# Performance work log

Hardware: AMD Instinct MI355X
Metric: run time of the kernel (lower is better)

Reference implementation:

```python
import jax, jax.numpy as jnp
import numpy as np

NUM_HEADS = 32
NUM_KV_HEADS = 8
NUM_GROUPS = NUM_HEADS // NUM_KV_HEADS  # 4
HEAD_DIM = 64
HIDDEN = 2048
ROPE_THETA = 10000.0


def rotate_half(x):
    half = x.shape[-1] // 2
    x1, x2 = x[..., :half], x[..., half:]
    return jnp.concatenate([-x2, x1], axis=-1)


def rope_cos_sin(seq_len, dtype):
    inv_freq = 1.0 / (ROPE_THETA ** (jnp.arange(0, HEAD_DIM, 2, dtype=jnp.float32) / HEAD_DIM))
    pos = jnp.arange(seq_len, dtype=jnp.float32)
    freqs = jnp.outer(pos, inv_freq)          # [S, HEAD_DIM/2]
    emb = jnp.concatenate([freqs, freqs], axis=-1)  # [S, HEAD_DIM]
    return jnp.cos(emb).astype(dtype), jnp.sin(emb).astype(dtype)


def setup_inputs() -> dict:
    key = jax.random.key(0)
    k0, k1, k2, k3, k4 = jax.random.split(key, 5)
    B, S = 2, 2048
    scale = 0.02
    return {
        "hidden_states": jax.random.normal(k0, (B, S, HIDDEN), dtype=jnp.float32),
        "Wq": jax.random.normal(k1, (NUM_HEADS * HEAD_DIM, HIDDEN), dtype=jnp.float32) * scale,
        "Wk": jax.random.normal(k2, (NUM_KV_HEADS * HEAD_DIM, HIDDEN), dtype=jnp.float32) * scale,
        "Wv": jax.random.normal(k3, (NUM_KV_HEADS * HEAD_DIM, HIDDEN), dtype=jnp.float32) * scale,
        "Wo": jax.random.normal(k4, (HIDDEN, NUM_HEADS * HEAD_DIM), dtype=jnp.float32) * scale,
    }


def reference(hidden_states, Wq, Wk, Wv, Wo):
    B, S, _ = hidden_states.shape
    # projections (nn.Linear: x @ W.T)
    q = (hidden_states @ Wq.T).reshape(B, S, NUM_HEADS, HEAD_DIM).transpose(0, 2, 1, 3)
    k = (hidden_states @ Wk.T).reshape(B, S, NUM_KV_HEADS, HEAD_DIM).transpose(0, 2, 1, 3)
    v = (hidden_states @ Wv.T).reshape(B, S, NUM_KV_HEADS, HEAD_DIM).transpose(0, 2, 1, 3)

    cos, sin = rope_cos_sin(S, q.dtype)  # [S, HEAD_DIM]
    cos = cos[None, None]                # [1,1,S,HEAD_DIM]
    sin = sin[None, None]
    q = q * cos + rotate_half(q) * sin
    k = k * cos + rotate_half(k) * sin

    # GQA: repeat kv heads to match query heads (repeat_interleave on head dim)
    k = jnp.repeat(k, NUM_GROUPS, axis=1)  # [B, NUM_HEADS, S, HEAD_DIM]
    v = jnp.repeat(v, NUM_GROUPS, axis=1)

    scale = 1.0 / jnp.sqrt(jnp.asarray(HEAD_DIM, dtype=q.dtype))
    scores = jnp.einsum('bhqd,bhkd->bhqk', q, k) * scale  # [B,H,S,S]
    causal = jnp.tril(jnp.ones((S, S), dtype=bool))
    scores = jnp.where(causal[None, None], scores, jnp.asarray(-jnp.inf, dtype=scores.dtype))
    attn = jax.nn.softmax(scores, axis=-1)
    out = jnp.einsum('bhqk,bhkd->bhqd', attn, v)           # [B,H,S,D]
    out = out.transpose(0, 2, 1, 3).reshape(B, S, NUM_HEADS * HEAD_DIM)
    return out @ Wo.T
```

## Files before the change

kernel.cpp:

```cpp
#include <hip/hip_runtime.h>

#define S_LEN 2048
#define BATCH 2
#define NH 32
#define NKV 8
#define HD 64
#define HID 2048
#define NTOK (BATCH * S_LEN)
#define NQKV 3072
#define SC_Q 0.18033688011112042f

typedef __attribute__((ext_vector_type(8))) __bf16 bf16x8;
typedef __attribute__((ext_vector_type(4))) float f32x4;
typedef __attribute__((ext_vector_type(4))) float f32x4v;
typedef __attribute__((ext_vector_type(4))) ushort u16x4;

__device__ inline ushort f2b(float f) {
    union { float f; unsigned u; } x{f};
    unsigned r = (x.u + 0x7fff + ((x.u >> 16) & 1)) >> 16;
    return (ushort)r;
}
__device__ inline float b2f(ushort u) {
    union { unsigned u; float f; } x{(unsigned)u << 16};
    return x.f;
}
__device__ inline float ex2(float x) { return __builtin_amdgcn_exp2f(x); }

__global__ __launch_bounds__(256) void cvt_all(const float* __restrict__ hidden,
                                               const float* __restrict__ Wq,
                                               const float* __restrict__ Wk,
                                               const float* __restrict__ Wv,
                                               const float* __restrict__ Wo,
                                               ushort* __restrict__ hb,
                                               ushort* __restrict__ wqkv,
                                               ushort* __restrict__ wo) {
    for (int bid = blockIdx.x; bid < 18432; bid += gridDim.x) {
        const float* src;
        ushort* dst;
        int off;
        if (bid < 8192)        { src = hidden; dst = hb;                              off = bid; }
        else if (bid < 12288)  { src = Wq;     dst = wqkv;                            off = bid - 8192; }
        else if (bid < 13312)  { src = Wk;     dst = wqkv + (size_t)2048 * 2048;      off = bid - 12288; }
        else if (bid < 14336)  { src = Wv;     dst = wqkv + (size_t)2560 * 2048;      off = bid - 13312; }
        else                   { src = Wo;     dst = wo;                              off = bid - 14336; }
        size_t i = (size_t)off * 256 + threadIdx.x;
        f32x4v v = __builtin_nontemporal_load((const f32x4v*)src + i);
        u16x4 o = {f2b(v[0]), f2b(v[1]), f2b(v[2]), f2b(v[3])};
        *((u16x4*)dst + i) = o;
    }
}

__device__ inline void gl_lds16(const void* g, void* l) {
    __builtin_amdgcn_global_load_lds((const __attribute__((address_space(1))) void*)g,
                                     (__attribute__((address_space(3))) void*)l, 16, 0, 0);
}

__global__ __launch_bounds__(512, 2) void gemmQKV(const ushort* __restrict__ A,
                                                  const ushort* __restrict__ B,
                                                  ushort* __restrict__ Qd,
                                                  ushort* __restrict__ Kd,
                                                  ushort* __restrict__ Vd,
                                                  int M, int N, int K) {
    constexpr int CF = 3;
    constexpr int ABYTES = 256 * 64 * 2;
    constexpr int BBYTES = 192 * 64 * 2;
    __shared__ __align__(16) char lds[2][ABYTES + BBYTES];
    const int tid = threadIdx.x, lane = tid & 63, w = tid >> 6;
    const int wm = w >> 2, wn = w & 3, l15 = lane & 15, lg = lane >> 4;

    const int nbx = gridDim.x;
    int lid = blockIdx.y * nbx + blockIdx.x;
    const int cpx = (nbx * gridDim.y) >> 3;
    int swzb = (lid & 7) * cpx + (lid >> 3);
    const int m0 = (swzb / nbx) * 256, n0 = (swzb % nbx) * (CF * 64);

    const int srow = tid >> 3;
    const int scol = ((tid & 7) ^ (srow & 7)) * 8;
    const ushort* Ag = A + (size_t)(m0 + srow) * K + scol;
    const ushort* Bg = B + (size_t)(n0 + srow) * K + scol;

    auto stage = [&](int buf, int k0) {
        char* base = &lds[buf][0];
#pragma unroll
        for (int j = 0; j < CF; j++)
            gl_lds16(Bg + (size_t)(j * 64) * K + k0, base + ABYTES + (j * 64 + w * 8) * 128);
        gl_lds16(Ag + k0,                        base + (0 * 64 + w * 8) * 128);
        gl_lds16(Ag + (size_t)(2 * 64) * K + k0, base + (2 * 64 + w * 8) * 128);
        gl_lds16(Ag + (size_t)(1 * 64) * K + k0, base + (1 * 64 + w * 8) * 128);
        gl_lds16(Ag + (size_t)(3 * 64) * K + k0, base + (3 * 64 + w * 8) * 128);
    };

    f32x4 acc[8][CF] = {};

    stage(0, 0);

    const int NT = K >> 6;
    const int sw = (l15 & 7) * 16;
    const int po0 = (lg * 16) ^ sw, po1 = (64 + lg * 16) ^ sw;

    for (int t = 0; t < NT; ++t) {
        const char* pa = &lds[t & 1][0] + (wm * 128 + l15) * 128;
        const char* pb = &lds[t & 1][ABYTES] + (wn * CF * 16 + l15) * 128;

        asm volatile("s_waitcnt vmcnt(2)" ::: "memory");
        __builtin_amdgcn_s_barrier();
        __builtin_amdgcn_sched_barrier(0);
        if (t + 1 < NT) stage((t + 1) & 1, (t + 1) << 6);
        __builtin_amdgcn_sched_barrier(0);

        bf16x8 bf_[2][CF];
#pragma unroll
        for (int j = 0; j < CF; j++) {
            bf_[0][j] = *(const bf16x8*)(pb + j * 2048 + po0);
            bf_[1][j] = *(const bf16x8*)(pb + j * 2048 + po1);
        }
        bf16x8 a_[2][4];
#pragma unroll
        for (int i = 0; i < 4; i++) {
            a_[0][i] = *(const bf16x8*)(pa + i * 2048 + po0);
            a_[1][i] = *(const bf16x8*)(pa + i * 2048 + po1);
        }
        __builtin_amdgcn_s_setprio(1);
#pragma unroll
        for (int ks = 0; ks < 2; ks++)
#pragma unroll
            for (int i = 0; i < 4; i++)
#pragma unroll
                for (int j = 0; j < CF; j++)
                    acc[i][j] = __builtin_amdgcn_mfma_f32_16x16x32_bf16(a_[ks][i], bf_[ks][j], acc[i][j], 0, 0, 0);
        __builtin_amdgcn_s_setprio(0);

        if (t < NT - 1) asm volatile("s_waitcnt vmcnt(7)" ::: "memory");
        else            asm volatile("s_waitcnt vmcnt(0)" ::: "memory");
        __builtin_amdgcn_s_barrier();
        __builtin_amdgcn_sched_barrier(0);

        bf16x8 c_[2][4];
#pragma unroll
        for (int i = 0; i < 4; i++) {
            c_[0][i] = *(const bf16x8*)(pa + (4 + i) * 2048 + po0);
            c_[1][i] = *(const bf16x8*)(pa + (4 + i) * 2048 + po1);
        }
        __builtin_amdgcn_s_setprio(1);
#pragma unroll
        for (int ks = 0; ks < 2; ks++)
#pragma unroll
            for (int i = 0; i < 4; i++)
#pragma unroll
                for (int j = 0; j < CF; j++)
                    acc[4 + i][j] = __builtin_amdgcn_mfma_f32_16x16x32_bf16(c_[ks][i], bf_[ks][j], acc[4 + i][j], 0, 0, 0);
        __builtin_amdgcn_s_setprio(0);
    }

    const int mr = m0 + wm * 128 + lg * 4;
#pragma unroll
    for (int j = 0; j < CF; j++) {
        int cb = n0 + wn * CF * 16 + j * 16;
        ushort* dst;
        int dstride, colb;
        if (cb < 2048)      { dst = Qd; dstride = 2048; colb = cb + l15; }
        else if (cb < 2560) { dst = Kd; dstride = 512;  colb = cb - 2048 + l15; }
        else                { dst = Vd; dstride = 512;  colb = cb - 2560 + l15; }
#pragma unroll
        for (int i = 0; i < 8; i++)
#pragma unroll
            for (int r = 0; r < 4; r++)
                dst[(size_t)(mr + i * 16 + r) * dstride + colb] = f2b(acc[i][j][r]);
    }
}

__global__ __launch_bounds__(512, 2) void gemmO(const ushort* __restrict__ A,
                                                const ushort* __restrict__ B,
                                                float* __restrict__ C,
                                                int M, int N, int K) {
    constexpr int ABYTES = 128 * 64 * 2;
    constexpr int BBYTES = 256 * 64 * 2;
    __shared__ __align__(16) char lds[2][ABYTES + BBYTES];
    const int tid = threadIdx.x, lane = tid & 63, w = tid >> 6;
    const int wm = w >> 2, wn = w & 3, l15 = lane & 15, lg = lane >> 4;

    const int nbx = gridDim.x;
    int lid = blockIdx.y * nbx + blockIdx.x;
    const int cpx = (nbx * gridDim.y) >> 3;
    int swzb = (lid & 7) * cpx + (lid >> 3);
    const int m0 = (swzb / nbx) * 128, n0 = (swzb % nbx) * 256;

    const int srow = tid >> 3;
    const int scol = ((tid & 7) ^ (srow & 7)) * 8;
    const ushort* Ag = A + (size_t)(m0 + srow) * K + scol;
    const ushort* Bg = B + (size_t)(n0 + srow) * K + scol;

    auto stage = [&](int buf, int k0) {
        char* base = &lds[buf][0];
        gl_lds16(Ag + k0,                   base + (w * 8) * 128);
        gl_lds16(Ag + (size_t)64 * K + k0,  base + (64 + w * 8) * 128);
#pragma unroll
        for (int j = 0; j < 4; j++)
            gl_lds16(Bg + (size_t)(j * 64) * K + k0, base + ABYTES + (j * 64 + w * 8) * 128);
    };

    f32x4 acc[4][4] = {};

    stage(0, 0);
    stage(1, 64);

    const int NT = K >> 6;
    const int sw = (l15 & 7) * 16;
    const int po0 = (lg * 16) ^ sw, po1 = (64 + lg * 16) ^ sw;

    for (int t = 0; t < NT; ++t) {
        if (t < NT - 1) asm volatile("s_waitcnt vmcnt(6)" ::: "memory");
        else            asm volatile("s_waitcnt vmcnt(0)" ::: "memory");
        __builtin_amdgcn_s_barrier();
        __builtin_amdgcn_sched_barrier(0);

        const char* pa = &lds[t & 1][0] + (wm * 64 + l15) * 128;
        const char* pb = &lds[t & 1][ABYTES] + (wn * 64 + l15) * 128;

        bf16x8 a_[2][4], b_[2][4];
#pragma unroll
        for (int i = 0; i < 4; i++) {
            a_[0][i] = *(const bf16x8*)(pa + i * 2048 + po0);
            a_[1][i] = *(const bf16x8*)(pa + i * 2048 + po1);
            b_[0][i] = *(const bf16x8*)(pb + i * 2048 + po0);
            b_[1][i] = *(const bf16x8*)(pb + i * 2048 + po1);
        }
        __builtin_amdgcn_s_setprio(1);
#pragma unroll
        for (int ks = 0; ks < 2; ks++)
#pragma unroll
            for (int i = 0; i < 4; i++)
#pragma unroll
                for (int j = 0; j < 4; j++)
                    acc[i][j] = __builtin_amdgcn_mfma_f32_16x16x32_bf16(a_[ks][i], b_[ks][j], acc[i][j], 0, 0, 0);
        __builtin_amdgcn_s_setprio(0);

        __builtin_amdgcn_sched_barrier(0);
        __builtin_amdgcn_s_barrier();
        __builtin_amdgcn_sched_barrier(0);
        if (t + 2 < NT) stage(t & 1, (t + 2) << 6);
    }

    const int mr = m0 + wm * 64 + lg * 4, nc = n0 + wn * 64 + l15;
#pragma unroll
    for (int i = 0; i < 4; i++)
#pragma unroll
        for (int j = 0; j < 4; j++)
#pragma unroll
            for (int r = 0; r < 4; r++)
                C[(size_t)(mr + i * 16 + r) * N + nc + j * 16] = acc[i][j][r];
}

__global__ __launch_bounds__(256) void rope_k(ushort* __restrict__ Kb) {
    int idx = blockIdx.x * 256 + threadIdx.x;
    int t = idx >> 5, rem = idx & 31;
    int hh = rem >> 2, q8 = rem & 3;
    float pos = (float)(t & (S_LEN - 1));
    ushort* base = Kb + (size_t)t * 512 + hh * 64 + q8 * 8;
    ushort4 v0 = *(ushort4*)base, v1 = *(ushort4*)(base + 4);
    ushort4 u0 = *(ushort4*)(base + 32), u1 = *(ushort4*)(base + 36);
    ushort lo[8] = {v0.x, v0.y, v0.z, v0.w, v1.x, v1.y, v1.z, v1.w};
    ushort hi[8] = {u0.x, u0.y, u0.z, u0.w, u1.x, u1.y, u1.z, u1.w};
#pragma unroll
    for (int e = 0; e < 8; e++) {
        float f = ex2(-(float)(q8 * 8 + e) * 0.4152410118609203f);
        float sv, cv;
        __sincosf(pos * f, &sv, &cv);
        float x1 = b2f(lo[e]), x2 = b2f(hi[e]);
        lo[e] = f2b(x1 * cv - x2 * sv);
        hi[e] = f2b(x2 * cv + x1 * sv);
    }
    *(ushort4*)base        = make_ushort4(lo[0], lo[1], lo[2], lo[3]);
    *(ushort4*)(base + 4)  = make_ushort4(lo[4], lo[5], lo[6], lo[7]);
    *(ushort4*)(base + 32) = make_ushort4(hi[0], hi[1], hi[2], hi[3]);
    *(ushort4*)(base + 36) = make_ushort4(hi[4], hi[5], hi[6], hi[7]);
}

__global__ __launch_bounds__(256) void transpose_v(const ushort* __restrict__ V,
                                                   ushort* __restrict__ Vt) {
    __shared__ ushort tile[32][33];
    int bz = blockIdx.z, b = bz >> 3, kvh = bz & 7;
    int s0 = blockIdx.x * 32, d0 = blockIdx.y * 32;
    int tx = threadIdx.x & 31, ty = threadIdx.x >> 5;
#pragma unroll
    for (int i = 0; i < 4; i++)
        tile[ty + i * 8][tx] = V[(size_t)(b * S_LEN + s0 + ty + i * 8) * 512 + kvh * 64 + d0 + tx];
    __syncthreads();
#pragma unroll
    for (int i = 0; i < 4; i++)
        Vt[((size_t)((b * 8 + kvh) * 64 + d0 + ty + i * 8)) * S_LEN + s0 + tx] = tile[tx][ty + i * 8];
}

__global__ __launch_bounds__(256) void attn_k(const ushort* __restrict__ Q,
                                              const ushort* __restrict__ Kc,
                                              const ushort* __restrict__ Vt,
                                              ushort* __restrict__ O) {
    __shared__ __align__(16) ushort K_lds[3][4096];
    __shared__ __align__(16) ushort V_lds[3][4096];
    const int lane = threadIdx.x & 63, w = threadIdx.x >> 6;
    const int l15 = lane & 15, lg = lane >> 4;

    int lid = blockIdx.y * 8 + blockIdx.x;
    int swz = (lid & 7) * 64 + (lid >> 3);
    const int ps = swz & 7;
    const int bh = swz >> 3;
    const int b = bh >> 5, h = bh & 31, kvh = h >> 2;

    const ushort* kSrc[2];
    const ushort* vSrc[2];
    int dstU[2];
#pragma unroll
    for (int j = 0; j < 2; j++) {
        int u = w * 2 + j;
        int row = u * 8 + (lane >> 3);
        int po = (lane & 7) * 16;
        int fr = ((row & 3) | (((row >> 3) & 1) << 2)) << 4;
        int dus = (po ^ fr) >> 1;
        kSrc[j] = Kc + (size_t)(b * S_LEN + row) * 512 + kvh * 64 + dus;
        vSrc[j] = Vt + ((size_t)((b * 8 + kvh) * 64 + row)) * S_LEN + dus;
        dstU[j] = u * 512;
    }

    int fr_k = ((l15 & 3) | (((l15 >> 2) & 1) << 2)) << 4;
    int kbase = 1024 * (l15 >> 2) + 128 * (l15 & 3) + ((lg * 16) ^ (fr_k & 48));
    int k6 = (fr_k >> 6) & 1;
    int kb0 = kbase + 64 * k6, kb1 = kbase + 64 * (1 - k6);
    int fr_v = ((l15 & 3) | (((l15 >> 3) & 1) << 2)) << 4;
    int vbase = 128 * l15 + ((lg * 16) ^ (fr_v & 48));
    int v6 = (fr_v >> 6) & 1;
    int vb0 = vbase + 64 * v6, vb1 = vbase + 64 * (1 - v6);

    bf16x8 onesf;
#pragma unroll
    for (int i = 0; i < 8; i++) onesf[i] = (__bf16)1.0f;

    auto ropeq = [&](bf16x8& q0, bf16x8& q1, int qrow) {
        float pos = (float)qrow;
#pragma unroll
        for (int e = 0; e < 8; e++) {
            float f = ex2(-(float)(lg * 8 + e) * 0.4152410118609203f);
            float sv, cv;
            __sincosf(pos * f, &sv, &cv);
            float x1 = (float)q0[e], x2 = (float)q1[e];
            q0[e] = (__bf16)((x1 * cv - x2 * sv) * SC_Q);
            q1[e] = (__bf16)((x2 * cv + x1 * sv) * SC_Q);
        }
    };

    for (int half = 0; half < 2; ++half) {
        const int pp = half ? (15 - ps) : ps;
        const int q0A = pp * 128 + w * 16, q0B = q0A + 64;
        const int qrowA = q0A + l15, qrowB = q0B + l15;
        const int ktA = 2 * pp, ktB = 2 * pp + 1;

        const ushort* qpA = Q + (size_t)(b * S_LEN + qrowA) * HID + h * 64 + lg * 8;
        const ushort* qpB = Q + (size_t)(b * S_LEN + qrowB) * HID + h * 64 + lg * 8;
        bf16x8 qfA0 = *(const bf16x8*)qpA, qfA1 = *(const bf16x8*)(qpA + 32);
        bf16x8 qfB0 = *(const bf16x8*)qpB, qfB1 = *(const bf16x8*)(qpB + 32);
        ropeq(qfA0, qfA1, qrowA);
        ropeq(qfB0, qfB1, qrowB);
        asm volatile("s_waitcnt vmcnt(0)" ::: "memory");

        f32x4 aoA[4] = {}, aoB[4] = {};
        f32x4 lsumA = {}, lsumB = {};

        int i0 = 0, i1 = 1, i2 = 2;
#pragma unroll
        for (int j = 0; j < 2; j++) {
            gl_lds16(kSrc[j], &K_lds[0][dstU[j]]);
            gl_lds16(vSrc[j], &V_lds[0][dstU[j]]);
        }
#pragma unroll
        for (int j = 0; j < 2; j++) {
            gl_lds16(kSrc[j] + (size_t)64 * 512, &K_lds[1][dstU[j]]);
            gl_lds16(vSrc[j] + 64, &V_lds[1][dstU[j]]);
        }

        for (int kt = 0; kt <= ktB; ++kt) {
            const int kn = kt << 6;
            if (kt < ktB) asm volatile("s_waitcnt vmcnt(4)" ::: "memory");
            else          asm volatile("s_waitcnt vmcnt(0)" ::: "memory");
            __builtin_amdgcn_s_barrier();

            if (kt + 2 <= ktB) {
                const int kn2 = kn + 128;
#pragma unroll
                for (int j = 0; j < 2; j++) {
                    gl_lds16(kSrc[j] + (size_t)kn2 * 512, &K_lds[i2][dstU[j]]);
                    gl_lds16(vSrc[j] + kn2, &V_lds[i2][dstU[j]]);
                }
            }

            const char* Kt = (const char*)&K_lds[i0][0];
            const char* Vl = (const char*)&V_lds[i0][0];
            const bool aAct = (kt <= ktA);

            bf16x8 kf0[4], kf1[4];
#pragma unroll
            for (int kc = 0; kc < 4; kc++) {
                const int kcst = 4096 * (kc >> 1) + 512 * (kc & 1);
                kf0[kc] = *(const bf16x8*)(Kt + kb0 + kcst);
                kf1[kc] = *(const bf16x8*)(Kt + kb1 + kcst);
            }

            f32x4 sB[4], sA[4];
#pragma unroll
            for (int kc = 0; kc < 4; kc++) {
                f32x4 z = {};
                z = __builtin_amdgcn_mfma_f32_16x16x32_bf16(kf0[kc], qfB0, z, 0, 0, 0);
                z = __builtin_amdgcn_mfma_f32_16x16x32_bf16(kf1[kc], qfB1, z, 0, 0, 0);
                sB[kc] = z;
            }
            if (aAct) {
#pragma unroll
                for (int kc = 0; kc < 4; kc++) {
                    f32x4 z = {};
                    z = __builtin_amdgcn_mfma_f32_16x16x32_bf16(kf0[kc], qfA0, z, 0, 0, 0);
                    z = __builtin_amdgcn_mfma_f32_16x16x32_bf16(kf1[kc], qfA1, z, 0, 0, 0);
                    sA[kc] = z;
                }
            }

            if (kt == ktB) {
#pragma unroll
                for (int kc = 0; kc < 4; kc++)
#pragma unroll
                    for (int r = 0; r < 4; r++) {
                        int kv = kn + ((kc >> 1) << 5) + (lg << 3) + ((kc & 1) << 2) + r;
                        sB[kc][r] = (kv <= qrowB) ? sB[kc][r] : -INFINITY;
                    }
            }
            if (kt == ktA) {
#pragma unroll
                for (int kc = 0; kc < 4; kc++)
#pragma unroll
                    for (int r = 0; r < 4; r++) {
                        int kv = kn + ((kc >> 1) << 5) + (lg << 3) + ((kc & 1) << 2) + r;
                        sA[kc][r] = (kv <= qrowA) ? sA[kc][r] : -INFINITY;
                    }
            }

            bf16x8 pB0, pB1, pA0, pA1;
#pragma unroll
            for (int r = 0; r < 4; r++) {
                pB0[r]     = (__bf16)ex2(sB[0][r]);
                pB0[4 + r] = (__bf16)ex2(sB[1][r]);
                pB1[r]     = (__bf16)ex2(sB[2][r]);
                pB1[4 + r] = (__bf16)ex2(sB[3][r]);
            }
            if (aAct) {
#pragma unroll
                for (int r = 0; r < 4; r++) {
                    pA0[r]     = (__bf16)ex2(sA[0][r]);
                    pA0[4 + r] = (__bf16)ex2(sA[1][r]);
                    pA1[r]     = (__bf16)ex2(sA[2][r]);
                    pA1[4 + r] = (__bf16)ex2(sA[3][r]);
                }
            }

            lsumB = __builtin_amdgcn_mfma_f32_16x16x32_bf16(pB0, onesf, lsumB, 0, 0, 0);
            lsumB = __builtin_amdgcn_mfma_f32_16x16x32_bf16(pB1, onesf, lsumB, 0, 0, 0);
            if (aAct) {
                lsumA = __builtin_amdgcn_mfma_f32_16x16x32_bf16(pA0, onesf, lsumA, 0, 0, 0);
                lsumA = __builtin_amdgcn_mfma_f32_16x16x32_bf16(pA1, onesf, lsumA, 0, 0, 0);
            }

#pragma unroll
            for (int dt = 0; dt < 4; dt++) {
                bf16x8 vf0 = *(const bf16x8*)(Vl + vb0 + dt * 2048);
                bf16x8 vf1 = *(const bf16x8*)(Vl + vb1 + dt * 2048);
                aoB[dt] = __builtin_amdgcn_mfma_f32_16x16x32_bf16(pB0, vf0, aoB[dt], 0, 0, 0);
                aoB[dt] = __builtin_amdgcn_mfma_f32_16x16x32_bf16(pB1, vf1, aoB[dt], 0, 0, 0);
                if (aAct) {
                    aoA[dt] = __builtin_amdgcn_mfma_f32_16x16x32_bf16(pA0, vf0, aoA[dt], 0, 0, 0);
                    aoA[dt] = __builtin_amdgcn_mfma_f32_16x16x32_bf16(pA1, vf1, aoA[dt], 0, 0, 0);
                }
            }

            int t = i0; i0 = i1; i1 = i2; i2 = t;
        }

        float invA[4], invB[4];
#pragma unroll
        for (int r = 0; r < 4; r++) { invA[r] = 1.0f / lsumA[r]; invB[r] = 1.0f / lsumB[r]; }
        ushort* obA = O + (size_t)(b * S_LEN + q0A + lg * 4) * HID + h * 64 + l15;
        ushort* obB = O + (size_t)(b * S_LEN + q0B + lg * 4) * HID + h * 64 + l15;
#pragma unroll
        for (int dt = 0; dt < 4; dt++)
#pragma unroll
            for (int r = 0; r < 4; r++) {
                union { __bf16 h; ushort u; } cA{(__bf16)(aoA[dt][r] * invA[r])};
                union { __bf16 h; ushort u; } cB{(__bf16)(aoB[dt][r] * invB[r])};
                obA[(size_t)r * HID + dt * 16] = cA.u;
                obB[(size_t)r * HID + dt * 16] = cB.u;
            }

        __builtin_amdgcn_s_barrier();
    }
}

extern "C" void kernel_launch(void* const* d_in, const int* in_sizes, int n_in,
                              void* d_out, int out_size, void* d_ws, size_t ws_size,
                              hipStream_t stream) {
    const float* hidden = (const float*)d_in[0];
    const float* Wq = (const float*)d_in[1];
    const float* Wk = (const float*)d_in[2];
    const float* Wv = (const float*)d_in[3];
    const float* Wo = (const float*)d_in[4];

    char* ws = (char*)d_ws;
    size_t off = 0;
    auto alloc = [&](size_t bytes) -> void* {
        void* p = ws + off;
        off += (bytes + 255) & ~(size_t)255;
        return p;
    };
    ushort* hb   = (ushort*)alloc((size_t)NTOK * HID * 2);
    ushort* wqkv = (ushort*)alloc((size_t)NQKV * 2048 * 2);
    ushort* wo   = (ushort*)alloc((size_t)2048 * 2048 * 2);
    ushort* Qb   = (ushort*)alloc((size_t)NTOK * 2048 * 2);
    ushort* Kb   = (ushort*)alloc((size_t)NTOK * 512 * 2);
    ushort* Vb   = (ushort*)alloc((size_t)NTOK * 512 * 2);
    ushort* Vtb  = (ushort*)alloc((size_t)NTOK * 512 * 2);
    ushort* AO   = (ushort*)alloc((size_t)NTOK * 2048 * 2);

    cvt_all<<<2304, 256, 0, stream>>>(hidden, Wq, Wk, Wv, Wo, hb, wqkv, wo);

    gemmQKV<<<dim3(16, 16), 512, 0, stream>>>(hb, wqkv, Qb, Kb, Vb, NTOK, NQKV, 2048);

    rope_k<<<(NTOK * 32) / 256, 256, 0, stream>>>(Kb);

    transpose_v<<<dim3(S_LEN / 32, 2, BATCH * NKV), 256, 0, stream>>>(Vb, Vtb);

    attn_k<<<dim3(8, BATCH * NH), 256, 0, stream>>>(Qb, Kb, Vtb, AO);

    gemmO<<<dim3(8, 32), 512, 0, stream>>>(AO, wo, (float*)d_out, NTOK, 2048, 2048);
}
```

Measured before the change: 166.8 us.

## Restructure GEMM pipelines: single-phase QKV loop and triple-buffered O-projection

The QKV GEMM main loop drops its split two-phase schedule, which waited on partial A loads. It now waits for all loads, issues the next stage's prefetch, and runs all 8 A-row fragments in one MFMA block. This takes one barrier out of each iteration but raises register pressure (16 A fragments live) and removes the overlap of the second A half's load with compute. The O-projection GEMM moves from two to three rotating LDS buffers, issuing the t+2 prefetch right after the top barrier and dropping the end-of-iteration barrier, at the cost of more LDS per block that may reduce occupancy.

```diff
diff --git a/kernel.cpp b/kernel.cpp
--- a/kernel.cpp
+++ b/kernel.cpp
@@ -84,10 +84,9 @@
 #pragma unroll
         for (int j = 0; j < CF; j++)
             gl_lds16(Bg + (size_t)(j * 64) * K + k0, base + ABYTES + (j * 64 + w * 8) * 128);
-        gl_lds16(Ag + k0,                        base + (0 * 64 + w * 8) * 128);
-        gl_lds16(Ag + (size_t)(2 * 64) * K + k0, base + (2 * 64 + w * 8) * 128);
-        gl_lds16(Ag + (size_t)(1 * 64) * K + k0, base + (1 * 64 + w * 8) * 128);
-        gl_lds16(Ag + (size_t)(3 * 64) * K + k0, base + (3 * 64 + w * 8) * 128);
+#pragma unroll
+        for (int j = 0; j < 4; j++)
+            gl_lds16(Ag + (size_t)(j * 64) * K + k0, base + (j * 64 + w * 8) * 128);
     };
 
     f32x4 acc[8][CF] = {};
@@ -99,24 +98,24 @@
     const int po0 = (lg * 16) ^ sw, po1 = (64 + lg * 16) ^ sw;
 
     for (int t = 0; t < NT; ++t) {
-        const char* pa = &lds[t & 1][0] + (wm * 128 + l15) * 128;
-        const char* pb = &lds[t & 1][ABYTES] + (wn * CF * 16 + l15) * 128;
-
-        asm volatile("s_waitcnt vmcnt(2)" ::: "memory");
+        asm volatile("s_waitcnt vmcnt(0)" ::: "memory");
         __builtin_amdgcn_s_barrier();
         __builtin_amdgcn_sched_barrier(0);
         if (t + 1 < NT) stage((t + 1) & 1, (t + 1) << 6);
         __builtin_amdgcn_sched_barrier(0);
 
+        const char* pa = &lds[t & 1][0] + (wm * 128 + l15) * 128;
+        const char* pb = &lds[t & 1][ABYTES] + (wn * CF * 16 + l15) * 128;
+
         bf16x8 bf_[2][CF];
 #pragma unroll
         for (int j = 0; j < CF; j++) {
             bf_[0][j] = *(const bf16x8*)(pb + j * 2048 + po0);
             bf_[1][j] = *(const bf16x8*)(pb + j * 2048 + po1);
         }
-        bf16x8 a_[2][4];
-#pragma unroll
-        for (int i = 0; i < 4; i++) {
+        bf16x8 a_[2][8];
+#pragma unroll
+        for (int i = 0; i < 8; i++) {
             a_[0][i] = *(const bf16x8*)(pa + i * 2048 + po0);
             a_[1][i] = *(const bf16x8*)(pa + i * 2048 + po1);
         }
@@ -124,31 +123,10 @@
 #pragma unroll
         for (int ks = 0; ks < 2; ks++)
 #pragma unroll
-            for (int i = 0; i < 4; i++)
+            for (int i = 0; i < 8; i++)
 #pragma unroll
                 for (int j = 0; j < CF; j++)
                     acc[i][j] = __builtin_amdgcn_mfma_f32_16x16x32_bf16(a_[ks][i], bf_[ks][j], acc[i][j], 0, 0, 0);
-        __builtin_amdgcn_s_setprio(0);
-
-        if (t < NT - 1) asm volatile("s_waitcnt vmcnt(7)" ::: "memory");
-        else            asm volatile("s_waitcnt vmcnt(0)" ::: "memory");
-        __builtin_amdgcn_s_barrier();
-        __builtin_amdgcn_sched_barrier(0);
-
-        bf16x8 c_[2][4];
-#pragma unroll
-        for (int i = 0; i < 4; i++) {
-            c_[0][i] = *(const bf16x8*)(pa + (4 + i) * 2048 + po0);
-            c_[1][i] = *(const bf16x8*)(pa + (4 + i) * 2048 + po1);
-        }
-        __builtin_amdgcn_s_setprio(1);
-#pragma unroll
-        for (int ks = 0; ks < 2; ks++)
-#pragma unroll
-            for (int i = 0; i < 4; i++)
-#pragma unroll
-                for (int j = 0; j < CF; j++)
-                    acc[4 + i][j] = __builtin_amdgcn_mfma_f32_16x16x32_bf16(c_[ks][i], bf_[ks][j], acc[4 + i][j], 0, 0, 0);
         __builtin_amdgcn_s_setprio(0);
     }
 
@@ -175,7 +153,7 @@
                                                 int M, int N, int K) {
     constexpr int ABYTES = 128 * 64 * 2;
     constexpr int BBYTES = 256 * 64 * 2;
-    __shared__ __align__(16) char lds[2][ABYTES + BBYTES];
+    __shared__ __align__(16) char lds[3][ABYTES + BBYTES];
     const int tid = threadIdx.x, lane = tid & 63, w = tid >> 6;
     const int wm = w >> 2, wn = w & 3, l15 = lane & 15, lg = lane >> 4;
 
@@ -208,14 +186,17 @@
     const int sw = (l15 & 7) * 16;
     const int po0 = (lg * 16) ^ sw, po1 = (64 + lg * 16) ^ sw;
 
+    int i0 = 0, i1 = 1, i2 = 2;
     for (int t = 0; t < NT; ++t) {
         if (t < NT - 1) asm volatile("s_waitcnt vmcnt(6)" ::: "memory");
         else            asm volatile("s_waitcnt vmcnt(0)" ::: "memory");
         __builtin_amdgcn_s_barrier();
         __builtin_amdgcn_sched_barrier(0);
-
-        const char* pa = &lds[t & 1][0] + (wm * 64 + l15) * 128;
-        const char* pb = &lds[t & 1][ABYTES] + (wn * 64 + l15) * 128;
+        if (t + 2 < NT) stage(i2, (t + 2) << 6);
+        __builtin_amdgcn_sched_barrier(0);
+
+        const char* pa = &lds[i0][0] + (wm * 64 + l15) * 128;
+        const char* pb = &lds[i0][ABYTES] + (wn * 64 + l15) * 128;
 
         bf16x8 a_[2][4], b_[2][4];
 #pragma unroll
@@ -235,10 +216,7 @@
                     acc[i][j] = __builtin_amdgcn_mfma_f32_16x16x32_bf16(a_[ks][i], b_[ks][j], acc[i][j], 0, 0, 0);
         __builtin_amdgcn_s_setprio(0);
 
-        __builtin_amdgcn_sched_barrier(0);
-        __builtin_amdgcn_s_barrier();
-        __builtin_amdgcn_sched_barrier(0);
-        if (t + 2 < NT) stage(t & 1, (t + 2) << 6);
+        int tt = i0; i0 = i1; i1 = i2; i2 = tt;
     }
 
     const int mr = m0 + wm * 64 + lg * 4, nc = n0 + wn * 64 + l15;
```

Result: faster. 160.8 us (-3.6%).
